# Kernel optimization log

Hardware: AMD Instinct MI355X
Metric: run time of the kernel (lower is better)

## Reference

```python
import jax, jax.numpy as jnp
import numpy as np

B, S, D = 2, 2048, 2048
HQ, HKV, HD = 16, 8, 128
F = 8192
V = 32000
L = 2
SW = 512
SOFTCAP = 50.0
THETA = 10000.0
EPS = 1e-6
LAYER_TYPES = ("sliding_attention", "full_attention")
SCALE = HD ** -0.5


def _rms_norm(x, w):
    # Gemma-style RMSNorm: fp32 compute, (1 + weight) scale
    x32 = x.astype(jnp.float32)
    n = x32 * jax.lax.rsqrt(jnp.mean(x32 * x32, axis=-1, keepdims=True) + EPS)
    return (n * (1.0 + w.astype(jnp.float32))).astype(x.dtype)


def _rotate_half(x):
    x1, x2 = jnp.split(x, 2, axis=-1)
    return jnp.concatenate([-x2, x1], axis=-1)


def _rope_cos_sin(position_ids):
    inv_freq = 1.0 / (THETA ** (jnp.arange(0, HD, 2, dtype=jnp.float32) / HD))  # [HD/2]
    freqs = position_ids.astype(jnp.float32)[..., None] * inv_freq  # [B,S,HD/2]
    emb = jnp.concatenate([freqs, freqs], axis=-1)  # [B,S,HD]
    return jnp.cos(emb), jnp.sin(emb)


def _apply_rope(q, k, cos, sin):
    # q,k: [B,H,S,HD]; cos,sin: [B,S,HD] -> unsqueeze head dim
    c, s = cos[:, None], sin[:, None]
    return q * c + _rotate_half(q) * s, k * c + _rotate_half(k) * s


def _build_masks(attention_mask, position_ids):
    key_mask = attention_mask.astype(bool)  # [B,S]
    # segment ids from position resets (packed sequences)
    boundaries = (position_ids[:, 1:] <= position_ids[:, :-1]).astype(jnp.int32)
    seg = jnp.cumsum(jnp.concatenate([jnp.ones((B, 1), jnp.int32), boundaries], axis=1), axis=1)
    block = seg[:, :, None] == seg[:, None, :]  # [B,S,S]
    full = (key_mask[:, None, :] & block)[:, None]  # [B,1,S,S]
    rows = jnp.arange(S)
    dist = rows[:, None] - rows[None, :]
    left = (SW + 1) // 2
    right = SW // 2 + 1
    window = ((dist >= 0) & (dist < left)) | ((dist < 0) & (-dist < right))
    sliding = full & window[None, None]
    return {"full_attention": full, "sliding_attention": sliding}


def _attention(x, l, wq, wk, wv, wo, q_norm_w, k_norm_w, cos, sin, mask):
    q = jnp.einsum("bsd,dhe->bhse", x, wq[l].reshape(D, HQ, HD))
    k = jnp.einsum("bsd,dhe->bhse", x, wk[l].reshape(D, HKV, HD))
    v = jnp.einsum("bsd,dhe->bhse", x, wv[l].reshape(D, HKV, HD))
    q = _rms_norm(q, q_norm_w[l])
    k = _rms_norm(k, k_norm_w[l])
    q, k = _apply_rope(q, k, cos, sin)
    rep = HQ // HKV
    k = jnp.repeat(k, rep, axis=1)  # repeat_kv
    v = jnp.repeat(v, rep, axis=1)
    scores = jnp.einsum("bhqd,bhkd->bhqk", q, k) * SCALE
    scores = jnp.tanh(scores / SOFTCAP) * SOFTCAP  # logit softcapping
    big_neg = jnp.finfo(jnp.float32).min
    scores = jnp.where(mask, scores, big_neg)
    probs = jax.nn.softmax(scores.astype(jnp.float32), axis=-1).astype(x.dtype)
    out = jnp.einsum("bhqk,bhkd->bhqd", probs, v)
    out = out.transpose(0, 2, 1, 3).reshape(B, S, HQ * HD)
    return out @ wo[l]


def _mlp(x, l, w_gate_up, w_down):
    gu = x @ w_gate_up[l]
    gate, up = jnp.split(gu, 2, axis=-1)
    return (jax.nn.gelu(gate, approximate=True) * up) @ w_down[l]


def setup_inputs() -> dict:
    key = jax.random.key(0)
    ks = jax.random.split(key, 12)
    w = lambda k, shape: (jax.random.normal(k, shape, jnp.float32) * 0.02)
    inp = {
        "embed": w(ks[0], (V, D)),
        "wq": w(ks[1], (L, D, HQ * HD)),
        "wk": w(ks[2], (L, D, HKV * HD)),
        "wv": w(ks[3], (L, D, HKV * HD)),
        "wo": w(ks[4], (L, HQ * HD, D)),
        "q_norm_w": jnp.zeros((L, HD), jnp.float32),
        "k_norm_w": jnp.zeros((L, HD), jnp.float32),
        "ln_in": jnp.zeros((L, D), jnp.float32),
        "ln_post_attn": jnp.zeros((L, D), jnp.float32),
        "ln_pre_ffn": jnp.zeros((L, D), jnp.float32),
        "ln_post_ffn": jnp.zeros((L, D), jnp.float32),
        "w_gate_up": w(ks[5], (L, D, 2 * F)),
        "w_down": w(ks[6], (L, F, D)),
        "final_norm_w": jnp.zeros((D,), jnp.float32),
        "input_ids": jax.random.randint(ks[7], (B, S), 0, V, jnp.int32),
        "attention_mask": jnp.ones((B, S), jnp.int32),
        # packed sequences: positions reset at the midpoint of each row
        "position_ids": jnp.broadcast_to(
            jnp.concatenate([jnp.arange(S // 2), jnp.arange(S - S // 2)]).astype(jnp.int32)[None, :],
            (B, S),
        ),
    }
    return inp


def reference(embed, wq, wk, wv, wo, q_norm_w, k_norm_w, ln_in, ln_post_attn,
              ln_pre_ffn, ln_post_ffn, w_gate_up, w_down, final_norm_w,
              input_ids, attention_mask, position_ids):
    masks = _build_masks(attention_mask, position_ids)
    cos, sin = _rope_cos_sin(position_ids)
    # scaled word embedding (Gemma style)
    x = embed[input_ids] * jnp.asarray(D ** 0.5, embed.dtype)
    for l in range(L):
        mask = masks[LAYER_TYPES[l]]
        h = _rms_norm(x, ln_in[l])
        h = _attention(h, l, wq, wk, wv, wo, q_norm_w, k_norm_w, cos, sin, mask)
        x = x + _rms_norm(h, ln_post_attn[l])
        h = _rms_norm(x, ln_pre_ffn[l])
        h = _mlp(h, l, w_gate_up, w_down)
        x = x + _rms_norm(h, ln_post_ffn[l])
    return _rms_norm(x, final_norm_w)
```

## Files before the change

kernel.cpp:

```cpp
#include <hip/hip_runtime.h>
#include <cstdint>
#include <cstddef>

typedef __bf16 bf16x8 __attribute__((ext_vector_type(8)));
typedef float  f32x4  __attribute__((ext_vector_type(4)));

#define BATCH 2
#define SEQ   2048
#define DMODEL 2048
#define NHQ   16
#define NHKV  8
#define HDIM  128
#define FFDIM 8192
#define NTOK  4096

__device__ __forceinline__ f32x4 mfma16(bf16x8 a, bf16x8 b, f32x4 c) {
    return __builtin_amdgcn_mfma_f32_16x16x32_bf16(a, b, c, 0, 0, 0);
}

__device__ __forceinline__ void gload16(const __bf16* g, __bf16* l) {
    __builtin_amdgcn_global_load_lds(
        (const __attribute__((address_space(1))) void*)g,
        (__attribute__((address_space(3))) void*)l, 16, 0, 0);
}

__device__ inline float wave_sum64(float v) {
    v += __shfl_xor(v, 1);  v += __shfl_xor(v, 2);  v += __shfl_xor(v, 4);
    v += __shfl_xor(v, 8);  v += __shfl_xor(v, 16); v += __shfl_xor(v, 32);
    return v;
}

__device__ inline float block_sum256(float v, float* lds4) {
    v = wave_sum64(v);
    const int w = threadIdx.x >> 6;
    __syncthreads();
    if ((threadIdx.x & 63) == 0) lds4[w] = v;
    __syncthreads();
    return lds4[0] + lds4[1] + lds4[2] + lds4[3];
}

__device__ __forceinline__ float softcap_exp(float s_raw) {
    const float K1 = 0.08838834764831845f * 0.04f;
    float u = __expf(s_raw * K1);
    return __expf(50.f - 100.f * __builtin_amdgcn_rcpf(1.f + u));
}

__global__ void transpose_cvt(const float* __restrict__ src, __bf16* __restrict__ dst,
                              int K, int N) {
    __shared__ float tile[32][33];
    const int tx = threadIdx.x, ty = threadIdx.y;
    const int n0 = blockIdx.x * 32, k0 = blockIdx.y * 32;
    #pragma unroll
    for (int i = 0; i < 4; ++i)
        tile[ty + i * 8][tx] = src[(size_t)(k0 + ty + i * 8) * N + n0 + tx];
    __syncthreads();
    #pragma unroll
    for (int i = 0; i < 4; ++i)
        dst[(size_t)(n0 + ty + i * 8) * K + k0 + tx] = (__bf16)tile[tx][ty + i * 8];
}

__global__ void transpose_cvt_gu(const float* __restrict__ src, __bf16* __restrict__ dst,
                                 int K, int N) {
    __shared__ float tile[32][33];
    const int tx = threadIdx.x, ty = threadIdx.y;
    const int n0 = blockIdx.x * 32, k0 = blockIdx.y * 32;
    #pragma unroll
    for (int i = 0; i < 4; ++i)
        tile[ty + i * 8][tx] = src[(size_t)(k0 + ty + i * 8) * N + n0 + tx];
    __syncthreads();
    #pragma unroll
    for (int i = 0; i < 4; ++i) {
        int n = n0 + ty + i * 8;
        int rI;
        if (n < 8192) rI = ((n & ~15) << 1) + (n & 15);
        else { int u = n - 8192; rI = ((u & ~15) << 1) + 16 + (u & 15); }
        dst[(size_t)rI * K + k0 + tx] = (__bf16)tile[tx][ty + i * 8];
    }
}

__global__ void transpose_bf16_k(const __bf16* __restrict__ src0, __bf16* __restrict__ dst0,
                                 int R, int C) {
    __shared__ __bf16 tile[32][34];
    const int z = blockIdx.z;
    const __bf16* src = src0 + (size_t)z * R * C;
    __bf16* dst = dst0 + (size_t)z * R * C;
    const int tx = threadIdx.x, ty = threadIdx.y;
    const int c0 = blockIdx.x * 32, r0 = blockIdx.y * 32;
    #pragma unroll
    for (int i = 0; i < 4; ++i)
        tile[ty + i * 8][tx] = src[(size_t)(r0 + ty + i * 8) * C + c0 + tx];
    __syncthreads();
    #pragma unroll
    for (int i = 0; i < 4; ++i)
        dst[(size_t)(c0 + ty + i * 8) * R + r0 + tx] = tile[tx][ty + i * 8];
}

__global__ __launch_bounds__(256) void embed_k(const float* __restrict__ emb,
                                               const int* __restrict__ ids,
                                               float* __restrict__ x) {
    const int row = blockIdx.x, t = threadIdx.x;
    const int id = ids[row];
    const size_t src = (size_t)id * DMODEL, dst = (size_t)row * DMODEL;
    const float sc = 45.2548339959390f;
    float4 a = *(const float4*)&emb[src + t * 4];
    float4 b = *(const float4*)&emb[src + t * 4 + 1024];
    a.x *= sc; a.y *= sc; a.z *= sc; a.w *= sc;
    b.x *= sc; b.y *= sc; b.z *= sc; b.w *= sc;
    *(float4*)&x[dst + t * 4] = a;
    *(float4*)&x[dst + t * 4 + 1024] = b;
}

__global__ __launch_bounds__(256) void seg_scan(const int* __restrict__ pos,
                                                int* __restrict__ seg) {
    __shared__ int wsum[4];
    const int b = blockIdx.x, t = threadIdx.x;
    const int lane = t & 63, wv = t >> 6;
    const int base = b * SEQ;
    int f[8]; int loc = 0;
    #pragma unroll
    for (int i = 0; i < 8; ++i) {
        int s = t * 8 + i;
        int fl = (s > 0) ? (pos[base + s] <= pos[base + s - 1]) : 0;
        f[i] = fl; loc += fl;
    }
    int sc = loc;
    for (int o = 1; o < 64; o <<= 1) { int n = __shfl_up(sc, o); if (lane >= o) sc += n; }
    if (lane == 63) wsum[wv] = sc;
    __syncthreads();
    int wb = 0;
    for (int i = 0; i < wv; ++i) wb += wsum[i];
    int run = wb + sc - loc + 1;
    #pragma unroll
    for (int i = 0; i < 8; ++i) { run += f[i]; seg[base + t * 8 + i] = run; }
}

template<int MODE, int NH>
__global__ __launch_bounds__(256) void fused_norm_k(
        float* __restrict__ x, const float* __restrict__ hA, const float* __restrict__ hB,
        const float* __restrict__ wA, const float* __restrict__ wB,
        __bf16* __restrict__ outb, float* __restrict__ outf) {
    __shared__ float lds4[4];
    const int row = blockIdx.x, t = threadIdx.x;
    const size_t base = (size_t)row * DMODEL;
    const int c0 = t * 4, c1 = t * 4 + 1024;
    float v[8];
    if constexpr (MODE == 0) {
        float4 a = *(const float4*)&x[base + c0];
        float4 b = *(const float4*)&x[base + c1];
        v[0]=a.x; v[1]=a.y; v[2]=a.z; v[3]=a.w;
        v[4]=b.x; v[5]=b.y; v[6]=b.z; v[7]=b.w;
    } else {
        float4 ha = *(const float4*)&hA[base + c0];
        float4 hb = *(const float4*)&hA[base + c1];
        float hv[8] = {ha.x, ha.y, ha.z, ha.w, hb.x, hb.y, hb.z, hb.w};
        if constexpr (NH == 2) {
            float4 ga = *(const float4*)&hB[base + c0];
            float4 gb = *(const float4*)&hB[base + c1];
            hv[0]+=ga.x; hv[1]+=ga.y; hv[2]+=ga.z; hv[3]+=ga.w;
            hv[4]+=gb.x; hv[5]+=gb.y; hv[6]+=gb.z; hv[7]+=gb.w;
        }
        float ss = 0.f;
        #pragma unroll
        for (int i = 0; i < 8; ++i) ss += hv[i] * hv[i];
        float tot = block_sum256(ss, lds4);
        float rs = rsqrtf(tot * (1.f / DMODEL) + 1e-6f);
        float4 xa = *(const float4*)&x[base + c0];
        float4 xb = *(const float4*)&x[base + c1];
        float xv[8] = {xa.x, xa.y, xa.z, xa.w, xb.x, xb.y, xb.z, xb.w};
        #pragma unroll
        for (int i = 0; i < 8; ++i) {
            int c = (i < 4) ? c0 + i : c1 + i - 4;
            v[i] = xv[i] + hv[i] * rs * (1.f + wA[c]);
        }
        float4 o0 = {v[0], v[1], v[2], v[3]}, o1 = {v[4], v[5], v[6], v[7]};
        *(float4*)&x[base + c0] = o0;
        *(float4*)&x[base + c1] = o1;
    }
    float ss2 = 0.f;
    #pragma unroll
    for (int i = 0; i < 8; ++i) ss2 += v[i] * v[i];
    float tot2 = block_sum256(ss2, lds4);
    float rs2 = rsqrtf(tot2 * (1.f / DMODEL) + 1e-6f);
    #pragma unroll
    for (int i = 0; i < 8; ++i) {
        int c = (i < 4) ? c0 + i : c1 + i - 4;
        float o = v[i] * rs2 * (1.f + wB[c]);
        if constexpr (MODE == 2) outf[base + c] = o;
        else outb[base + c] = (__bf16)o;
    }
}

template<int MH, int NH>
__device__ __forceinline__ void quad(f32x4 (&acc)[8][4], const bf16x8 (&af)[4][2],
                                     const bf16x8 (&bfr)[2][2]) {
    #pragma unroll
    for (int mq = 0; mq < 4; ++mq)
        #pragma unroll
        for (int nq = 0; nq < 2; ++nq)
            #pragma unroll
            for (int ks = 0; ks < 2; ++ks)
                acc[MH*4+mq][NH*2+nq] = mfma16(af[mq][ks], bfr[nq][ks], acc[MH*4+mq][NH*2+nq]);
}

template<typename OutT, int GELU>
__global__ __launch_bounds__(512, 2) void gemm8p(const __bf16* __restrict__ A,
                                                 const __bf16* __restrict__ Bw,
                                                 OutT* __restrict__ C,
                                                 int M, int N, int Ksub, int lda, int ldb) {
    __shared__ __bf16 lds[65536];
    const int z = blockIdx.z;
    A += (size_t)z * Ksub;
    Bw += (size_t)z * Ksub;
    C += (size_t)z * M * N;

    const int nx = gridDim.x;
    const int ny = gridDim.y;
    const int nwg = nx * ny;
    const int orig = blockIdx.y * nx + blockIdx.x;
    const int wg = ((nwg & 7) == 0) ? ((orig & 7) * (nwg >> 3) + (orig >> 3)) : orig;
    const int gsize = 8 * nx;
    const int gid = wg / gsize;
    const int first_m = gid * 8;
    const int rows = min(8, ny - first_m);
    const int loc = wg - gid * gsize;
    const int bm = (first_m + loc % rows) * 256;
    const int bn = (loc / rows) * 256;

    const int t = threadIdx.x;
    const int w = t >> 6, lane = t & 63;
    const int wm = w >> 2, wn = w & 3;
    const int lg = lane >> 4, lr = lane & 15;

    const int rS = t >> 3, sS = t & 7;
    const int colS = ((sS ^ (rS & 7)) << 3);
    const __bf16* Ag = A + (size_t)(bm + rS) * lda + colS;
    const __bf16* Bg = Bw + (size_t)(bn + rS) * ldb + colS;
    const int nt = Ksub >> 6;

#define STAGE_A(kt, h) { \
        const __bf16* g_ = Ag + (size_t)(h) * 128 * lda + (size_t)(kt) * 64; \
        const int li_ = (((kt) & 1) << 15) + ((h) << 13) + t * 8; \
        gload16(g_, &lds[li_]); \
        gload16(g_ + (size_t)64 * lda, &lds[li_ + 4096]); }
#define STAGE_B(kt, h) { \
        const __bf16* g_ = Bg + (size_t)(h) * 128 * ldb + (size_t)(kt) * 64; \
        const int li_ = (((kt) & 1) << 15) + 16384 + ((h) << 13) + t * 8; \
        gload16(g_, &lds[li_]); \
        gload16(g_ + (size_t)64 * ldb, &lds[li_ + 4096]); }

    f32x4 acc[8][4] = {};
    bf16x8 af[4][2], bf0[2][2], bf1[2][2];

    const int swz = (lr & 7) << 3;
    const int aBase = wm * 8192;
    const int bBase = 16384 + (wn >> 1) * 8192;
    const int bRow0 = (wn & 1) * 64;
    const int lo0 = (lg * 8) ^ swz;
    const int lo1 = (32 + lg * 8) ^ swz;

#define RD_A(bufv, rowoff) { \
        _Pragma("unroll") \
        for (int mq = 0; mq < 4; ++mq) { \
            const int rb_ = (bufv) + aBase + ((rowoff) + mq * 16 + lr) * 64; \
            af[mq][0] = *(const bf16x8*)&lds[rb_ + lo0]; \
            af[mq][1] = *(const bf16x8*)&lds[rb_ + lo1]; } }
#define RD_B0(bufv) { \
        _Pragma("unroll") \
        for (int nq = 0; nq < 2; ++nq) { \
            const int rb_ = (bufv) + bBase + (bRow0 + nq * 16 + lr) * 64; \
            bf0[nq][0] = *(const bf16x8*)&lds[rb_ + lo0]; \
            bf0[nq][1] = *(const bf16x8*)&lds[rb_ + lo1]; } }
#define RD_B1(bufv) { \
        _Pragma("unroll") \
        for (int nq = 0; nq < 2; ++nq) { \
            const int rb_ = (bufv) + bBase + (bRow0 + 32 + nq * 16 + lr) * 64; \
            bf1[nq][0] = *(const bf16x8*)&lds[rb_ + lo0]; \
            bf1[nq][1] = *(const bf16x8*)&lds[rb_ + lo1]; } }

    STAGE_A(0, 0); STAGE_A(0, 1); STAGE_B(0, 0); STAGE_B(0, 1);
    if (nt > 1) {
        STAGE_A(1, 0); STAGE_A(1, 1); STAGE_B(1, 0); STAGE_B(1, 1);
        asm volatile("s_waitcnt vmcnt(8)" ::: "memory");
    } else {
        asm volatile("s_waitcnt vmcnt(0)" ::: "memory");
    }
    __builtin_amdgcn_s_barrier();
    asm volatile("" ::: "memory");
    RD_A(0, 0);
    RD_B0(0);

    for (int kt = 0; kt < nt; ++kt) {
        const int buf = (kt & 1) << 15;
        const int obuf = buf ^ (1 << 15);
        const bool p1 = (kt + 1 < nt), p2 = (kt + 2 < nt);
        RD_B1(buf);
        asm volatile("s_waitcnt lgkmcnt(4)" ::: "memory");
        __builtin_amdgcn_sched_barrier(0);
        __builtin_amdgcn_s_setprio(1);
        quad<0,0>(acc, af, bf0);
        __builtin_amdgcn_s_setprio(0);
        __builtin_amdgcn_s_barrier();
        asm volatile("" ::: "memory");
        asm volatile("s_waitcnt lgkmcnt(0)" ::: "memory");
        __builtin_amdgcn_sched_barrier(0);
        __builtin_amdgcn_s_setprio(1);
        quad<0,1>(acc, af, bf1);
        __builtin_amdgcn_s_setprio(0);
        __builtin_amdgcn_sched_barrier(0);
        RD_A(buf, 64);
        asm volatile("s_waitcnt lgkmcnt(0)" ::: "memory");
        __builtin_amdgcn_s_barrier();
        asm volatile("" ::: "memory");
        if (p2) { STAGE_A(kt + 2, 0); STAGE_A(kt + 2, 1); }
        __builtin_amdgcn_sched_barrier(0);
        __builtin_amdgcn_s_setprio(1);
        quad<1,1>(acc, af, bf1);
        __builtin_amdgcn_s_setprio(0);
        __builtin_amdgcn_s_barrier();
        asm volatile("" ::: "memory");
        if (p2) {
            STAGE_B(kt + 2, 0); STAGE_B(kt + 2, 1);
            asm volatile("s_waitcnt vmcnt(8)" ::: "memory");
        } else if (p1) {
            asm volatile("s_waitcnt vmcnt(0)" ::: "memory");
        }
        __builtin_amdgcn_s_barrier();
        asm volatile("" ::: "memory");
        __builtin_amdgcn_sched_barrier(0);
        __builtin_amdgcn_s_setprio(1);
        quad<1,0>(acc, af, bf0);
        __builtin_amdgcn_s_setprio(0);
        __builtin_amdgcn_sched_barrier(0);
        if (p1) { RD_A(obuf, 0); RD_B0(obuf); }
        __builtin_amdgcn_s_barrier();
        asm volatile("" ::: "memory");
    }
#undef STAGE_A
#undef STAGE_B
#undef RD_A
#undef RD_B0
#undef RD_B1

    if constexpr (GELU) {
        const int nhalf = N >> 1;
        #pragma unroll
        for (int m = 0; m < 8; ++m)
            #pragma unroll
            for (int pp = 0; pp < 2; ++pp)
                #pragma unroll
                for (int r = 0; r < 4; ++r) {
                    float g = acc[m][2 * pp][r];
                    float u = acc[m][2 * pp + 1][r];
                    float a2 = 1.5957691216057308f * (g + 0.044715f * g * g * g);
                    float sig = __builtin_amdgcn_rcpf(1.f + __expf(-a2));
                    float res = g * sig * u;
                    const int row = bm + wm * 128 + m * 16 + lg * 4 + r;
                    const int col = (bn >> 1) + wn * 32 + pp * 16 + lr;
                    C[(size_t)row * nhalf + col] = (OutT)res;
                }
    } else {
        #pragma unroll
        for (int m = 0; m < 8; ++m)
            #pragma unroll
            for (int n = 0; n < 4; ++n)
                #pragma unroll
                for (int r = 0; r < 4; ++r) {
                    const int row = bm + wm * 128 + m * 16 + lg * 4 + r;
                    const int col = bn + wn * 64 + n * 16 + lr;
                    C[(size_t)row * N + col] = (OutT)acc[m][n][r];
                }
    }
}

__global__ __launch_bounds__(256) void qkv_post(const __bf16* __restrict__ qkv,
                                                const float* __restrict__ qnw,
                                                const float* __restrict__ knw,
                                                const int* __restrict__ posid,
                                                __bf16* __restrict__ qg,
                                                __bf16* __restrict__ kg,
                                                __bf16* __restrict__ vg) {
    const int slot = blockIdx.x * 4 + (threadIdx.x >> 6);
    const int lane = threadIdx.x & 63;
    const int token = slot >> 5, j = slot & 31;
    const int b = token >> 11, s = token & (SEQ - 1);
    int base;
    const float* nw = nullptr;
    if (j < 16)      { base = j * 128;                nw = qnw; }
    else if (j < 24) { base = 2048 + (j - 16) * 128;  nw = knw; }
    else             { base = 3072 + (j - 24) * 128; }
    float e0 = (float)qkv[(size_t)token * 4096 + base + lane];
    float e1 = (float)qkv[(size_t)token * 4096 + base + lane + 64];
    if (j < 24) {
        float ss = wave_sum64(e0 * e0 + e1 * e1);
        float rs = rsqrtf(ss * (1.f / 128.f) + 1e-6f);
        e0 *= rs * (1.f + nw[lane]);
        e1 *= rs * (1.f + nw[lane + 64]);
        float p = (float)posid[token];
        float inv = exp2f(-13.287712379549449f * ((float)lane * (1.f / 64.f)));
        float f = p * inv;
        float c = cosf(f), sn = sinf(f);
        float o0 = e0 * c - e1 * sn;
        float o1 = e1 * c + e0 * sn;
        e0 = o0; e1 = o1;
    }
    size_t dst; __bf16* out;
    if (j < 16)      { dst = ((size_t)(b * NHQ  + j)        * SEQ + s) * HDIM; out = qg; }
    else if (j < 24) { dst = ((size_t)(b * NHKV + (j - 16)) * SEQ + s) * HDIM; out = kg; }
    else             { dst = ((size_t)(b * NHKV + (j - 24)) * SEQ + s) * HDIM; out = vg; }
    out[dst + lane] = (__bf16)e0;
    out[dst + lane + 64] = (__bf16)e1;
}

template<int SLIDING>
__global__ __launch_bounds__(256, 2) void attn_k(const __bf16* __restrict__ qg,
                                                 const __bf16* __restrict__ kg,
                                                 const __bf16* __restrict__ vtg,
                                                 const int* __restrict__ seg,
                                                 const int* __restrict__ amask,
                                                 __bf16* __restrict__ outg) {
    __shared__ __align__(16) __bf16 Ks[64][136];
    __shared__ __align__(16) __bf16 Vs[128][72];
    __shared__ __align__(16) __bf16 Ps[4][16][72];
    __shared__ int segq_s[64], segk_s[64], kmk_s[64];
    __shared__ int flag_s;
    const int bh = blockIdx.y;
    const int b = bh >> 4, h = bh & 15, kvh = h >> 1;
    const int qb = blockIdx.x * 64;
    const int t = threadIdx.x, w = t >> 6, lane = t & 63;
    const int lg = lane >> 4, lr = lane & 15;
    const int segbase = b * SEQ;

    const size_t qoff = ((size_t)(b * NHQ + h) * SEQ + qb + w * 16) * HDIM;
    bf16x8 qf[4];
    #pragma unroll
    for (int kk = 0; kk < 4; ++kk)
        qf[kk] = *(const bf16x8*)&qg[qoff + (size_t)lr * HDIM + kk * 32 + lg * 8];
    if (t < 64) segq_s[t] = seg[segbase + qb + t];

    const int sqmin = seg[segbase + qb], sqmax = seg[segbase + qb + 63];

    const int krow = t >> 4, kcol = (t & 15) * 8;
    const int vrow = t >> 3, vcol = (t & 7) * 8;
    const __bf16* kB = kg + ((size_t)(b * NHKV + kvh) * SEQ) * HDIM + (size_t)krow * HDIM + kcol;
    const __bf16* vB = vtg + ((size_t)(b * NHKV + kvh) * HDIM + vrow) * SEQ + vcol;

    auto chunk_active = [&](int kb) -> bool {
        if (SLIDING && (qb - kb < -318 || qb - kb > 319)) return false;
        int skmin = seg[segbase + kb], skmax = seg[segbase + kb + 63];
        return (skmax >= sqmin) && (skmin <= sqmax);
    };
    auto next_kb = [&](int kb) -> int {
        for (kb += 64; kb < SEQ; kb += 64)
            if (chunk_active(kb)) return kb;
        return SEQ;
    };

    int4 kr0, kr1, kr2, kr3, vr0, vr1, vr2, vr3;
#define LOADR(kb_) { \
        kr0 = *(const int4*)(kB + (size_t)(kb_) * HDIM); \
        kr1 = *(const int4*)(kB + (size_t)((kb_) + 16) * HDIM); \
        kr2 = *(const int4*)(kB + (size_t)((kb_) + 32) * HDIM); \
        kr3 = *(const int4*)(kB + (size_t)((kb_) + 48) * HDIM); \
        vr0 = *(const int4*)(vB + (kb_)); \
        vr1 = *(const int4*)(vB + (size_t)32 * SEQ + (kb_)); \
        vr2 = *(const int4*)(vB + (size_t)64 * SEQ + (kb_)); \
        vr3 = *(const int4*)(vB + (size_t)96 * SEQ + (kb_)); }

    f32x4 oacc[8] = {};
    float den[4] = {0.f, 0.f, 0.f, 0.f};

    int kb = chunk_active(0) ? 0 : next_kb(0);
    if (kb < SEQ) LOADR(kb);

    while (kb < SEQ) {
        const int nkb = next_kb(kb);
        __syncthreads();
        *(int4*)&Ks[krow     ][kcol] = kr0;
        *(int4*)&Ks[krow + 16][kcol] = kr1;
        *(int4*)&Ks[krow + 32][kcol] = kr2;
        *(int4*)&Ks[krow + 48][kcol] = kr3;
        *(int4*)&Vs[vrow     ][vcol] = vr0;
        *(int4*)&Vs[vrow + 32][vcol] = vr1;
        *(int4*)&Vs[vrow + 64][vcol] = vr2;
        *(int4*)&Vs[vrow + 96][vcol] = vr3;
        if (w == 0) {
            int m = amask[segbase + kb + lane];
            int sk = seg[segbase + kb + lane];
            kmk_s[lane] = m; segk_s[lane] = sk;
            bool allm = (__ballot(m != 0) == ~0ull);
            bool segu = __all(sk == sqmin) && (sqmin == sqmax);
            bool wall = !SLIDING || (qb - kb >= -193 && qb - kb <= 192);
            if (lane == 0) flag_s = (allm && segu && wall) ? 1 : 0;
        }
        __syncthreads();
        if (nkb < SEQ) LOADR(nkb);
        const bool fast = (flag_s != 0);

        #pragma unroll
        for (int n = 0; n < 4; ++n) {
            f32x4 sc = {};
            #pragma unroll
            for (int kk = 0; kk < 4; ++kk) {
                bf16x8 bfr = *(const bf16x8*)&Ks[n * 16 + lr][kk * 32 + lg * 8];
                sc = mfma16(qf[kk], bfr, sc);
            }
            if (fast) {
                #pragma unroll
                for (int r = 0; r < 4; ++r) {
                    int row = lg * 4 + r;
                    float p = softcap_exp(sc[r]);
                    den[r] += p;
                    Ps[w][row][n * 16 + lr] = (__bf16)p;
                }
            } else {
                #pragma unroll
                for (int r = 0; r < 4; ++r) {
                    int row = lg * 4 + r;
                    int qi = qb + w * 16 + row;
                    int ki = kb + n * 16 + lr;
                    bool ok = (kmk_s[n * 16 + lr] != 0) &&
                              (segq_s[w * 16 + row] == segk_s[n * 16 + lr]);
                    if (SLIDING) { int d = qi - ki; ok = ok && (d >= -256) && (d <= 255); }
                    float p = ok ? softcap_exp(sc[r]) : 0.f;
                    den[r] += p;
                    Ps[w][row][n * 16 + lr] = (__bf16)p;
                }
            }
        }
        #pragma unroll
        for (int kk2 = 0; kk2 < 2; ++kk2) {
            bf16x8 pf = *(const bf16x8*)&Ps[w][lr][kk2 * 32 + lg * 8];
            #pragma unroll
            for (int n2 = 0; n2 < 8; ++n2) {
                bf16x8 vf = *(const bf16x8*)&Vs[n2 * 16 + lr][kk2 * 32 + lg * 8];
                oacc[n2] = mfma16(pf, vf, oacc[n2]);
            }
        }
        kb = nkb;
    }
#undef LOADR
    #pragma unroll
    for (int r = 0; r < 4; ++r) {
        float v = den[r];
        v += __shfl_xor(v, 1); v += __shfl_xor(v, 2);
        v += __shfl_xor(v, 4); v += __shfl_xor(v, 8);
        den[r] = __builtin_amdgcn_rcpf(v);
    }
    #pragma unroll
    for (int n2 = 0; n2 < 8; ++n2)
        #pragma unroll
        for (int r = 0; r < 4; ++r) {
            int row = qb + w * 16 + lg * 4 + r;
            float val = oacc[n2][r] * den[r];
            outg[((size_t)(b * SEQ) + row) * DMODEL + h * HDIM + n2 * 16 + lr] = (__bf16)val;
        }
}

extern "C" void kernel_launch(void* const* d_in, const int* in_sizes, int n_in,
                              void* d_out, int out_size, void* d_ws, size_t ws_size,
                              hipStream_t stream) {
    const float* embedw = (const float*)d_in[0];
    const float* wq   = (const float*)d_in[1];
    const float* wk   = (const float*)d_in[2];
    const float* wv   = (const float*)d_in[3];
    const float* wo   = (const float*)d_in[4];
    const float* qnw  = (const float*)d_in[5];
    const float* knw  = (const float*)d_in[6];
    const float* lnin = (const float*)d_in[7];
    const float* lnpa = (const float*)d_in[8];
    const float* lnpf = (const float*)d_in[9];
    const float* lnpff= (const float*)d_in[10];
    const float* wguW = (const float*)d_in[11];
    const float* wdnW = (const float*)d_in[12];
    const float* fnw  = (const float*)d_in[13];
    const int* ids    = (const int*)d_in[14];
    const int* amask  = (const int*)d_in[15];
    const int* posid  = (const int*)d_in[16];
    float* outp = (float*)d_out;

    char* ws = (char*)d_ws;
    size_t off = 0;
    auto A = [&](size_t b) -> char* {
        char* p = ws + off;
        off = (off + b + 255) & ~(size_t)255;
        return p;
    };
    __bf16* qkvwt = (__bf16*)A((size_t)4096 * 2048 * 2);
    __bf16* wot   = (__bf16*)A((size_t)2048 * 2048 * 2);
    __bf16* wgut  = (__bf16*)A((size_t)16384 * 2048 * 2);
    __bf16* wdnt  = (__bf16*)A((size_t)2048 * 8192 * 2);
    float*  x     = (float*)A((size_t)NTOK * DMODEL * 4);
    __bf16* hbuf  = (__bf16*)A((size_t)NTOK * DMODEL * 2);
    __bf16* qkvb  = (__bf16*)A((size_t)NTOK * 4096 * 2);
    __bf16* qbh   = (__bf16*)A((size_t)BATCH * NHQ  * SEQ * HDIM * 2);
    __bf16* kbh   = (__bf16*)A((size_t)BATCH * NHKV * SEQ * HDIM * 2);
    __bf16* vbh   = (__bf16*)A((size_t)BATCH * NHKV * SEQ * HDIM * 2);
    __bf16* vtbh  = (__bf16*)A((size_t)BATCH * NHKV * SEQ * HDIM * 2);
    __bf16* attnb = (__bf16*)A((size_t)NTOK * DMODEL * 2);
    __bf16* actb  = (__bf16*)A((size_t)NTOK * FFDIM * 2);
    float*  pbuf  = (float*)A((size_t)2 * NTOK * DMODEL * 4);
    int*    seg   = (int*)A((size_t)BATCH * SEQ * 4);
    if (off > ws_size) return;

    const dim3 tb(32, 8);
    seg_scan<<<BATCH, 256, 0, stream>>>(posid, seg);
    embed_k<<<NTOK, 256, 0, stream>>>(embedw, ids, x);
    fused_norm_k<0,1><<<NTOK, 256, 0, stream>>>(x, nullptr, nullptr, nullptr, lnin, hbuf, nullptr);

    for (int l = 0; l < 2; ++l) {
        transpose_cvt<<<dim3(64, 64), tb, 0, stream>>>(wq + (size_t)l * 2048 * 2048,
            qkvwt, 2048, 2048);
        transpose_cvt<<<dim3(32, 64), tb, 0, stream>>>(wk + (size_t)l * 2048 * 1024,
            qkvwt + (size_t)2048 * 2048, 2048, 1024);
        transpose_cvt<<<dim3(32, 64), tb, 0, stream>>>(wv + (size_t)l * 2048 * 1024,
            qkvwt + (size_t)3072 * 2048, 2048, 1024);
        transpose_cvt<<<dim3(64, 64), tb, 0, stream>>>(wo + (size_t)l * 2048 * 2048,
            wot, 2048, 2048);
        transpose_cvt_gu<<<dim3(512, 64), tb, 0, stream>>>(wguW + (size_t)l * 2048 * 16384,
            wgut, 2048, 16384);
        transpose_cvt<<<dim3(64, 256), tb, 0, stream>>>(wdnW + (size_t)l * 8192 * 2048,
            wdnt, 8192, 2048);

        gemm8p<__bf16,0><<<dim3(16, 16, 1), 512, 0, stream>>>(hbuf, qkvwt, qkvb,
                                                              4096, 4096, 2048, 2048, 2048);
        qkv_post<<<32768, 256, 0, stream>>>(qkvb, qnw + l * 128, knw + l * 128, posid,
                                            qbh, kbh, vbh);
        transpose_bf16_k<<<dim3(4, 64, BATCH * NHKV), tb, 0, stream>>>(vbh, vtbh, SEQ, HDIM);
        if (l == 0)
            attn_k<1><<<dim3(SEQ / 64, BATCH * NHQ), 256, 0, stream>>>(qbh, kbh, vtbh, seg,
                                                                       amask, attnb);
        else
            attn_k<0><<<dim3(SEQ / 64, BATCH * NHQ), 256, 0, stream>>>(qbh, kbh, vtbh, seg,
                                                                       amask, attnb);
        gemm8p<float,0><<<dim3(8, 16, 2), 512, 0, stream>>>(attnb, wot, pbuf,
                                                            4096, 2048, 1024, 2048, 2048);
        fused_norm_k<1,2><<<NTOK, 256, 0, stream>>>(x, pbuf, pbuf + (size_t)NTOK * DMODEL,
                                                    lnpa + l * 2048, lnpf + l * 2048,
                                                    hbuf, nullptr);
        gemm8p<__bf16,1><<<dim3(64, 16, 1), 512, 0, stream>>>(hbuf, wgut, actb,
                                                              4096, 16384, 2048, 2048, 2048);
        gemm8p<float,0><<<dim3(8, 16, 2), 512, 0, stream>>>(actb, wdnt, pbuf,
                                                            4096, 2048, 4096, 8192, 8192);
        if (l == 0)
            fused_norm_k<1,2><<<NTOK, 256, 0, stream>>>(x, pbuf, pbuf + (size_t)NTOK * DMODEL,
                                                        lnpff, lnin + 2048, hbuf, nullptr);
        else
            fused_norm_k<2,2><<<NTOK, 256, 0, stream>>>(x, pbuf, pbuf + (size_t)NTOK * DMODEL,
                                                        lnpff + 2048, fnw, nullptr, outp);
    }
}
```

Baseline: 1.458 ms.

## Restructure GEMM K-loop to prefetch one tile ahead with split staging

Reworks the GEMM main loop's global-to-LDS pipeline. Instead of prefetching two K-tiles ahead in whole A/B blocks, it prefetches only the next tile, split into quarter-sized loads interleaved between the four MFMA quadrants, with vmcnt waits and barriers placed per quadrant. The aim is to spread memory traffic more evenly across the compute phases and cut barrier count. In exchange, load latency is hidden by less lookahead, and the LDS reads for a tile are no longer issued ahead during the previous iteration.

Result: faster. 1.419 ms (-2.7%).

```diff
diff --git a/kernel.cpp b/kernel.cpp
--- a/kernel.cpp
+++ b/kernel.cpp
@@ -237,16 +237,12 @@
     const __bf16* Bg = Bw + (size_t)(bn + rS) * ldb + colS;
     const int nt = Ksub >> 6;
 
-#define STAGE_A(kt, h) { \
-        const __bf16* g_ = Ag + (size_t)(h) * 128 * lda + (size_t)(kt) * 64; \
-        const int li_ = (((kt) & 1) << 15) + ((h) << 13) + t * 8; \
-        gload16(g_, &lds[li_]); \
-        gload16(g_ + (size_t)64 * lda, &lds[li_ + 4096]); }
-#define STAGE_B(kt, h) { \
-        const __bf16* g_ = Bg + (size_t)(h) * 128 * ldb + (size_t)(kt) * 64; \
-        const int li_ = (((kt) & 1) << 15) + 16384 + ((h) << 13) + t * 8; \
-        gload16(g_, &lds[li_]); \
-        gload16(g_ + (size_t)64 * ldb, &lds[li_ + 4096]); }
+#define STAGE_AU(kt, h, s) { \
+        const __bf16* g_ = Ag + (size_t)((h) * 128 + (s) * 64) * lda + (size_t)(kt) * 64; \
+        gload16(g_, &lds[(((kt) & 1) << 15) + (h) * 8192 + (s) * 4096 + t * 8]); }
+#define STAGE_BU(kt, h, s) { \
+        const __bf16* g_ = Bg + (size_t)((h) * 128 + (s) * 64) * ldb + (size_t)(kt) * 64; \
+        gload16(g_, &lds[(((kt) & 1) << 15) + 16384 + (h) * 8192 + (s) * 4096 + t * 8]); }
 
     f32x4 acc[8][4] = {};
     bf16x8 af[4][2], bf0[2][2], bf1[2][2];
@@ -277,66 +273,59 @@
             bf1[nq][0] = *(const bf16x8*)&lds[rb_ + lo0]; \
             bf1[nq][1] = *(const bf16x8*)&lds[rb_ + lo1]; } }
 
-    STAGE_A(0, 0); STAGE_A(0, 1); STAGE_B(0, 0); STAGE_B(0, 1);
-    if (nt > 1) {
-        STAGE_A(1, 0); STAGE_A(1, 1); STAGE_B(1, 0); STAGE_B(1, 1);
-        asm volatile("s_waitcnt vmcnt(8)" ::: "memory");
-    } else {
-        asm volatile("s_waitcnt vmcnt(0)" ::: "memory");
-    }
-    __builtin_amdgcn_s_barrier();
-    asm volatile("" ::: "memory");
-    RD_A(0, 0);
-    RD_B0(0);
+    STAGE_BU(0, 0, 0); STAGE_BU(0, 0, 1); STAGE_BU(0, 1, 0); STAGE_BU(0, 1, 1);
+    STAGE_AU(0, 0, 0); STAGE_AU(0, 1, 0); STAGE_AU(0, 0, 1); STAGE_AU(0, 1, 1);
 
     for (int kt = 0; kt < nt; ++kt) {
         const int buf = (kt & 1) << 15;
-        const int obuf = buf ^ (1 << 15);
-        const bool p1 = (kt + 1 < nt), p2 = (kt + 2 < nt);
-        RD_B1(buf);
-        asm volatile("s_waitcnt lgkmcnt(4)" ::: "memory");
+        const bool p1 = (kt + 1 < nt);
+        if (p1) {
+            STAGE_BU(kt + 1, 0, 0); STAGE_BU(kt + 1, 0, 1);
+            asm volatile("s_waitcnt vmcnt(4)" ::: "memory");
+        } else {
+            asm volatile("s_waitcnt vmcnt(2)" ::: "memory");
+        }
+        __builtin_amdgcn_s_barrier();
+        asm volatile("" ::: "memory");
+        RD_A(buf, 0); RD_B0(buf);
+        asm volatile("s_waitcnt lgkmcnt(0)" ::: "memory");
         __builtin_amdgcn_sched_barrier(0);
         __builtin_amdgcn_s_setprio(1);
         quad<0,0>(acc, af, bf0);
         __builtin_amdgcn_s_setprio(0);
-        __builtin_amdgcn_s_barrier();
         asm volatile("" ::: "memory");
+        if (p1) { STAGE_BU(kt + 1, 1, 0); STAGE_BU(kt + 1, 1, 1); }
+        RD_B1(buf);
         asm volatile("s_waitcnt lgkmcnt(0)" ::: "memory");
         __builtin_amdgcn_sched_barrier(0);
         __builtin_amdgcn_s_setprio(1);
         quad<0,1>(acc, af, bf1);
         __builtin_amdgcn_s_setprio(0);
-        __builtin_amdgcn_sched_barrier(0);
+        asm volatile("" ::: "memory");
+        if (p1) {
+            STAGE_AU(kt + 1, 0, 0); STAGE_AU(kt + 1, 1, 0);
+            asm volatile("s_waitcnt vmcnt(6)" ::: "memory");
+        } else {
+            asm volatile("s_waitcnt vmcnt(0)" ::: "memory");
+        }
+        __builtin_amdgcn_s_barrier();
+        asm volatile("" ::: "memory");
         RD_A(buf, 64);
         asm volatile("s_waitcnt lgkmcnt(0)" ::: "memory");
-        __builtin_amdgcn_s_barrier();
-        asm volatile("" ::: "memory");
-        if (p2) { STAGE_A(kt + 2, 0); STAGE_A(kt + 2, 1); }
         __builtin_amdgcn_sched_barrier(0);
         __builtin_amdgcn_s_setprio(1);
         quad<1,1>(acc, af, bf1);
         __builtin_amdgcn_s_setprio(0);
-        __builtin_amdgcn_s_barrier();
         asm volatile("" ::: "memory");
-        if (p2) {
-            STAGE_B(kt + 2, 0); STAGE_B(kt + 2, 1);
-            asm volatile("s_waitcnt vmcnt(8)" ::: "memory");
-        } else if (p1) {
-            asm volatile("s_waitcnt vmcnt(0)" ::: "memory");
-        }
-        __builtin_amdgcn_s_barrier();
-        asm volatile("" ::: "memory");
+        if (p1) { STAGE_AU(kt + 1, 0, 1); STAGE_AU(kt + 1, 1, 1); }
         __builtin_amdgcn_sched_barrier(0);
         __builtin_amdgcn_s_setprio(1);
         quad<1,0>(acc, af, bf0);
         __builtin_amdgcn_s_setprio(0);
-        __builtin_amdgcn_sched_barrier(0);
-        if (p1) { RD_A(obuf, 0); RD_B0(obuf); }
-        __builtin_amdgcn_s_barrier();
         asm volatile("" ::: "memory");
     }
-#undef STAGE_A
-#undef STAGE_B
+#undef STAGE_AU
+#undef STAGE_BU
 #undef RD_A
 #undef RD_B0
 #undef RD_B1
```
